# Optimization experiments

Hardware: AMD Instinct MI355X
Metric: run time of the kernel (lower is better)

The kernel has to match this reference:

```python
import jax, jax.numpy as jnp
import numpy as np

N = 100000      # nodes
E = 800000      # edges (avg degree 8)
D_IN = 128
D_OUT = 128
HOPS = 3        # K in SGConv


def setup_inputs() -> dict:
    key = jax.random.key(0)
    k1, k2, k3 = jax.random.split(key, 3)
    x = jax.random.normal(k1, (N, D_IN), dtype=jnp.float32)
    edge_index = jax.random.randint(k2, (2, E), 0, N, dtype=jnp.int64)
    # SGConv's final torch.nn.Linear(in_channels, out_channels)
    W = jax.random.normal(k3, (D_OUT, D_IN), dtype=jnp.float32) / np.sqrt(D_IN).astype(np.float32)
    b = jnp.zeros((D_OUT,), dtype=jnp.float32)
    return {"x": x, "edge_index": edge_index, "W": W, "b": b}


def reference(x, edge_index, W, b):
    n = x.shape[0]
    loop = jnp.arange(n, dtype=edge_index.dtype)
    # gcn_norm with add_self_loops=True (SGConv default)
    src = jnp.concatenate([edge_index[0], loop])  # message sources
    dst = jnp.concatenate([edge_index[1], loop])  # aggregation targets
    ones = jnp.ones(src.shape[0], dtype=x.dtype)
    deg = jax.ops.segment_sum(ones, dst, num_segments=n)
    dinv = jnp.where(deg > 0, jax.lax.rsqrt(deg), 0.0)
    norm = dinv[src] * dinv[dst]  # symmetric D^-1/2 A_hat D^-1/2 coefficients

    def hop(h, _):
        msg = h[src] * norm[:, None]                      # [E+N, D] gather
        return jax.ops.segment_sum(msg, dst, num_segments=n), None

    h, _ = jax.lax.scan(hop, x, None, length=HOPS)        # A_norm^K x
    return h @ W.T + b                                     # final linear
```

## Files before the change

### kernel.cpp

```cpp
#include <hip/hip_runtime.h>
#include <hip/hip_bf16.h>

#define DF 128


typedef __attribute__((ext_vector_type(8))) short shortx8;
typedef __attribute__((ext_vector_type(4))) float floatx4;

__device__ __forceinline__ unsigned short f32_to_bf16_rne(float f) {
    unsigned int u = __float_as_uint(f);
    unsigned int r = (u >> 16) & 1u;
    u += 0x7FFFu + r;
    return (unsigned short)(u >> 16);
}
__device__ __forceinline__ float bf16_lo(unsigned int w) { return __uint_as_float(w << 16); }
__device__ __forceinline__ float bf16_hi(unsigned int w) { return __uint_as_float(w & 0xffff0000u); }
__device__ __forceinline__ unsigned int pack_bf16(float x, float y) {
    return ((unsigned int)f32_to_bf16_rne(y) << 16) | (unsigned int)f32_to_bf16_rne(x);
}

__global__ void detect_flags_kernel(const unsigned int* __restrict__ ew, int enwords,
                                    const unsigned short* __restrict__ xh, int xnh,
                                    int* __restrict__ flagI, int* __restrict__ flagD) {
    __shared__ int eodd_nz;
    __shared__ int xbig;
    if (threadIdx.x == 0) { eodd_nz = 0; xbig = 0; }
    __syncthreads();
    int f1 = 0;
    for (int i = 1 + 2 * (int)threadIdx.x; i < enwords; i += 2 * (int)blockDim.x)
        if (ew[i] != 0u) f1 = 1;
    int c = 0;
    for (int i = 2 * (int)threadIdx.x; i < xnh; i += 2 * (int)blockDim.x) {
        unsigned int e = ((unsigned int)xh[i] >> 7) & 0xFFu;
        if (e >= 0xC0u) c++;
    }
    if (f1) eodd_nz = 1;
    if (c) atomicAdd(&xbig, c);
    __syncthreads();
    if (threadIdx.x == 0) {
        *flagI = (eodd_nz == 0) ? 1 : 0;
        *flagD = (xbig > 8) ? 0 : 1;
    }
}

__global__ void count_deg_kernel(const int* __restrict__ eidx, const int* __restrict__ flagI,
                                 int E, int n, int* __restrict__ cnt) {
    int e = blockIdx.x * blockDim.x + threadIdx.x;
    if (e >= E) return;
    int s, d;
    if (*flagI) {
        const long long* p = (const long long*)eidx;
        s = (int)p[e];
        d = (int)p[(long long)E + e];
    } else {
        s = eidx[e];
        d = eidx[E + e];
    }
    if (d < 0 || d >= n || s < 0 || s >= n) return;
    atomicAdd(&cnt[d], 1);
}

__global__ void dinv_kernel(const int* __restrict__ cnt, float* __restrict__ dinv, int n) {
    int i = blockIdx.x * blockDim.x + threadIdx.x;
    if (i < n) dinv[i] = rsqrtf((float)(cnt[i] + 1));
}

__global__ void scan_blocks_kernel(const int* __restrict__ cnt, int* __restrict__ row_start,
                                   int* __restrict__ partials, int n) {
    __shared__ int s[256];
    int i = blockIdx.x * 256 + threadIdx.x;
    int v = (i < n) ? cnt[i] : 0;
    s[threadIdx.x] = v;
    __syncthreads();
    for (int off = 1; off < 256; off <<= 1) {
        int t = ((int)threadIdx.x >= off) ? s[threadIdx.x - off] : 0;
        __syncthreads();
        s[threadIdx.x] += t;
        __syncthreads();
    }
    if (i < n) row_start[i] = s[threadIdx.x] - v;
    if (threadIdx.x == 255) partials[blockIdx.x] = s[255];
}

__global__ void scan_partials_kernel(int* __restrict__ partials, int nparts) {
    __shared__ int s[512];
    int v = ((int)threadIdx.x < nparts) ? partials[threadIdx.x] : 0;
    s[threadIdx.x] = v;
    __syncthreads();
    for (int off = 1; off < 512; off <<= 1) {
        int t = ((int)threadIdx.x >= off) ? s[threadIdx.x - off] : 0;
        __syncthreads();
        s[threadIdx.x] += t;
        __syncthreads();
    }
    if ((int)threadIdx.x < nparts) partials[threadIdx.x] = s[threadIdx.x] - v;
}

__global__ void finalize_rows_kernel(int* __restrict__ row_start, const int* __restrict__ partials,
                                     const int* __restrict__ cnt, int* __restrict__ cursor, int n) {
    int i = blockIdx.x * 256 + threadIdx.x;
    if (i < n) {
        int r = row_start[i] + partials[blockIdx.x];
        row_start[i] = r;
        cursor[i] = r;
        if (i == n - 1) row_start[n] = r + cnt[i];
    }
}

__global__ void scatter_kernel(const int* __restrict__ eidx, const int* __restrict__ flagI,
                               int E, int n, const float* __restrict__ dinv,
                               int* __restrict__ cursor, int2* __restrict__ csr) {
    int e = blockIdx.x * blockDim.x + threadIdx.x;
    if (e >= E) return;
    int s, d;
    if (*flagI) {
        const long long* p = (const long long*)eidx;
        s = (int)p[e];
        d = (int)p[(long long)E + e];
    } else {
        s = eidx[e];
        d = eidx[E + e];
    }
    if (d < 0 || d >= n || s < 0 || s >= n) return;
    int pos = atomicAdd(&cursor[d], 1);
    int2 pk;
    pk.x = s;
    pk.y = __float_as_int(dinv[s]);
    csr[pos] = pk;
}

__global__ void cast_x_kernel(const void* __restrict__ x, uint2* __restrict__ xb,
                              const int* __restrict__ flagD, int nw2) {
    int i = blockIdx.x * blockDim.x + threadIdx.x;
    if (i >= nw2) return;
    if (*flagD) {
        xb[i] = ((const uint2*)x)[i];
    } else {
        float4 v = ((const float4*)x)[i];
        uint2 o;
        o.x = pack_bf16(v.x, v.y);
        o.y = pack_bf16(v.z, v.w);
        xb[i] = o;
    }
}

__global__ void cast_wb_kernel(const void* __restrict__ W, const void* __restrict__ b,
                               unsigned short* __restrict__ Wb, float* __restrict__ bias_f,
                               const int* __restrict__ flagD) {
    int i = blockIdx.x * 256 + threadIdx.x;
    int bf = *flagD;
    if (i < 128 * 128)
        Wb[i] = bf ? ((const unsigned short*)W)[i] : f32_to_bf16_rne(((const float*)W)[i]);
    if (i < 128)
        bias_f[i] = bf ? bf16_lo((unsigned int)((const unsigned short*)b)[i]) : ((const float*)b)[i];
}

__global__ __launch_bounds__(256) void hop_kernel(const uint4* __restrict__ hin,
                                                  uint4* __restrict__ hout,
                                                  const int2* __restrict__ csr,
                                                  const int* __restrict__ row_start,
                                                  const float* __restrict__ dinv, int n) {
    int gw = (int)((blockIdx.x * 256 + threadIdx.x) >> 6);
    int lane = (int)(threadIdx.x & 63);
    if (gw >= n) return;
    int e = lane >> 4, c = lane & 15;
    float di = dinv[gw];
    int beg = row_start[gw], end = row_start[gw + 1];
    uint4 sv = hin[(size_t)gw * 16 + c];
    float a0 = 0.f, a1 = 0.f, a2 = 0.f, a3 = 0.f, a4 = 0.f, a5 = 0.f, a6 = 0.f, a7 = 0.f;
    for (int j = beg + e; j < end; j += 4) {
        int2 ed = csr[j];
        float w = __int_as_float(ed.y);
        uint4 v = hin[(size_t)ed.x * 16 + c];
        a0 += w * bf16_lo(v.x); a1 += w * bf16_hi(v.x);
        a2 += w * bf16_lo(v.y); a3 += w * bf16_hi(v.y);
        a4 += w * bf16_lo(v.z); a5 += w * bf16_hi(v.z);
        a6 += w * bf16_lo(v.w); a7 += w * bf16_hi(v.w);
    }
    a0 += __shfl_xor(a0, 16); a0 += __shfl_xor(a0, 32);
    a1 += __shfl_xor(a1, 16); a1 += __shfl_xor(a1, 32);
    a2 += __shfl_xor(a2, 16); a2 += __shfl_xor(a2, 32);
    a3 += __shfl_xor(a3, 16); a3 += __shfl_xor(a3, 32);
    a4 += __shfl_xor(a4, 16); a4 += __shfl_xor(a4, 32);
    a5 += __shfl_xor(a5, 16); a5 += __shfl_xor(a5, 32);
    a6 += __shfl_xor(a6, 16); a6 += __shfl_xor(a6, 32);
    a7 += __shfl_xor(a7, 16); a7 += __shfl_xor(a7, 32);
    a0 = di * (a0 + di * bf16_lo(sv.x)); a1 = di * (a1 + di * bf16_hi(sv.x));
    a2 = di * (a2 + di * bf16_lo(sv.y)); a3 = di * (a3 + di * bf16_hi(sv.y));
    a4 = di * (a4 + di * bf16_lo(sv.z)); a5 = di * (a5 + di * bf16_hi(sv.z));
    a6 = di * (a6 + di * bf16_lo(sv.w)); a7 = di * (a7 + di * bf16_hi(sv.w));
    if (e == 0) {
        uint4 o;
        o.x = pack_bf16(a0, a1);
        o.y = pack_bf16(a2, a3);
        o.z = pack_bf16(a4, a5);
        o.w = pack_bf16(a6, a7);
        hout[(size_t)gw * 16 + c] = o;
    }
}

__global__ __launch_bounds__(256, 2) void linear_mfma_kernel(
        const unsigned short* __restrict__ h, const unsigned short* __restrict__ Wb,
        const float* __restrict__ bias_f, void* __restrict__ out,
        const int* __restrict__ flagD, int n) {
    int bf = *flagD;
    int wave = (int)(threadIdx.x >> 6);
    int lane = (int)(threadIdx.x & 63);
    int q = lane >> 4, m16 = lane & 15;

    shortx8 bfrag[8][4];
    float bias[8];
#pragma unroll
    for (int nt = 0; nt < 8; ++nt) {
        int wr = nt * 16 + m16;
#pragma unroll
        for (int t = 0; t < 4; ++t)
            bfrag[nt][t] = *(const shortx8*)&Wb[wr * 128 + t * 32 + q * 8];
        bias[nt] = bias_f[wr];
    }

    int nstrips = (n + 15) / 16;
    int wid = (int)blockIdx.x * 4 + wave;
    int nw = (int)gridDim.x * 4;
    for (int s = wid; s < nstrips; s += nw) {
        int row0 = s * 16;
        int arow = row0 + m16;
        if (arow >= n) arow = n - 1;
        shortx8 afrag[4];
#pragma unroll
        for (int t = 0; t < 4; ++t)
            afrag[t] = *(const shortx8*)&h[(size_t)arow * 128 + t * 32 + q * 8];

        floatx4 acc[8];
#pragma unroll
        for (int nt = 0; nt < 8; ++nt) acc[nt] = (floatx4){0.f, 0.f, 0.f, 0.f};
#pragma unroll
        for (int t = 0; t < 4; ++t)
#pragma unroll
            for (int nt = 0; nt < 8; ++nt)
                acc[nt] = __builtin_amdgcn_mfma_f32_16x16x32_bf16(afrag[t], bfrag[nt][t], acc[nt], 0, 0, 0);

#pragma unroll
        for (int nt = 0; nt < 8; ++nt)
#pragma unroll
            for (int r = 0; r < 4; ++r) {
                int row = row0 + q * 4 + r;
                if (row < n) {
                    float v = acc[nt][r] + bias[nt];
                    size_t oi = (size_t)row * 128 + nt * 16 + m16;
                    if (bf) ((unsigned short*)out)[oi] = f32_to_bf16_rne(v);
                    else    ((float*)out)[oi] = v;
                }
            }
    }
}

extern "C" void kernel_launch(void* const* d_in, const int* in_sizes, int n_in,
                              void* d_out, int out_size, void* d_ws, size_t ws_size,
                              hipStream_t stream) {
    const void* x = d_in[0];
    const int* eidx = (const int*)d_in[1];
    const void* W = d_in[2];
    const void* b = d_in[3];

    int n = in_sizes[0] / DF;
    int E = in_sizes[1] / 2;

    char* ws = (char*)d_ws;
    size_t off = 0;
    auto alloc = [&](size_t bytes) -> void* {
        void* p = ws + off;
        off = (off + bytes + 255) & ~(size_t)255;
        return p;
    };
    unsigned int* hb = (unsigned int*)alloc((size_t)n * 64 * 4);
    float* dinv      = (float*)alloc((size_t)n * 4);
    int*   cnt       = (int*)alloc((size_t)n * 4);
    int*   row_start = (int*)alloc((size_t)(n + 1) * 4);
    int*   cursor    = (int*)alloc((size_t)n * 4);
    int*   partials  = (int*)alloc(4096);
    int*   flagI     = (int*)alloc(256);
    int*   flagD     = (int*)alloc(256);
    unsigned short* Wb = (unsigned short*)alloc(128 * 128 * 2);
    float* bias_f    = (float*)alloc(128 * 4);
    int2*  csr       = (int2*)alloc((size_t)E * 8);
    unsigned int* xb = (unsigned int*)d_out;

    hipMemsetAsync(cnt, 0, (size_t)n * 4, stream);

    int enw = 8192; if (2 * E < enw) enw = 2 * E;
    int xnh = 16384; if (n * DF < xnh) xnh = n * DF;
    detect_flags_kernel<<<1, 256, 0, stream>>>((const unsigned int*)eidx, enw,
                                               (const unsigned short*)x, xnh, flagI, flagD);

    int eb = (E + 255) / 256;
    int nb = (n + 255) / 256;
    count_deg_kernel<<<eb, 256, 0, stream>>>(eidx, flagI, E, n, cnt);
    dinv_kernel<<<nb, 256, 0, stream>>>(cnt, dinv, n);
    scan_blocks_kernel<<<nb, 256, 0, stream>>>(cnt, row_start, partials, n);
    scan_partials_kernel<<<1, 512, 0, stream>>>(partials, nb);
    finalize_rows_kernel<<<nb, 256, 0, stream>>>(row_start, partials, cnt, cursor, n);
    scatter_kernel<<<eb, 256, 0, stream>>>(eidx, flagI, E, n, dinv, cursor, csr);

    int nw2 = n * 32;
    cast_x_kernel<<<(nw2 + 255) / 256, 256, 0, stream>>>(x, (uint2*)xb, flagD, nw2);
    cast_wb_kernel<<<64, 256, 0, stream>>>(W, b, Wb, bias_f, flagD);

    int hb_grid = (n + 3) / 4;
    hop_kernel<<<hb_grid, 256, 0, stream>>>((const uint4*)xb, (uint4*)hb, csr, row_start, dinv, n);
    hop_kernel<<<hb_grid, 256, 0, stream>>>((const uint4*)hb, (uint4*)xb, csr, row_start, dinv, n);
    hop_kernel<<<hb_grid, 256, 0, stream>>>((const uint4*)xb, (uint4*)hb, csr, row_start, dinv, n);

    int nstrips = (n + 15) / 16;
    int lgrid = 512; if ((nstrips + 3) / 4 < lgrid) lgrid = (nstrips + 3) / 4;
    linear_mfma_kernel<<<lgrid, 256, 0, stream>>>(
        (const unsigned short*)hb, Wb, bias_f, d_out, flagD, n);
}
```

Baseline: 358.5 us.

## Partition degree count and CSR scatter into destination-range buckets per block group

Count and scatter kernels now use a fixed grid of 512 blocks split into 8 groups. Each group loops over all edges but only handles destinations in its eighth of the node range. The aim is to localize atomics and CSR writes (likely keeping them within one XCD's L2 via block-to-XCD round robin) and cut cross-die atomic traffic. The cost is that each group rereads the whole destination index array, so index reads grow eightfold.

Measured after the change: 386.1 us. 7.7% more time.

```diff
diff --git a/kernel.cpp b/kernel.cpp
--- a/kernel.cpp
+++ b/kernel.cpp
@@ -43,21 +43,24 @@
     }
 }
 
-__global__ void count_deg_kernel(const int* __restrict__ eidx, const int* __restrict__ flagI,
-                                 int E, int n, int* __restrict__ cnt) {
-    int e = blockIdx.x * blockDim.x + threadIdx.x;
-    if (e >= E) return;
-    int s, d;
-    if (*flagI) {
-        const long long* p = (const long long*)eidx;
-        s = (int)p[e];
-        d = (int)p[(long long)E + e];
-    } else {
-        s = eidx[e];
-        d = eidx[E + e];
-    }
-    if (d < 0 || d >= n || s < 0 || s >= n) return;
-    atomicAdd(&cnt[d], 1);
+__global__ __launch_bounds__(256) void count_deg_kernel(const int* __restrict__ eidx,
+                                                        const int* __restrict__ flagI,
+                                                        int E, int n, int* __restrict__ cnt) {
+    int bucket = (int)(blockIdx.x & 7);
+    int bsize = (n + 7) >> 3;
+    int lo = bucket * bsize;
+    int hi = lo + bsize; if (hi > n) hi = n;
+    int nthr = (int)(gridDim.x >> 3) * (int)blockDim.x;
+    int t0 = (int)(blockIdx.x >> 3) * (int)blockDim.x + (int)threadIdx.x;
+    int isI64 = *flagI;
+    const long long* p64 = (const long long*)eidx;
+    for (int e = t0; e < E; e += nthr) {
+        int d = isI64 ? (int)p64[(long long)E + e] : eidx[E + e];
+        if (d < lo || d >= hi) continue;
+        int s = isI64 ? (int)p64[e] : eidx[e];
+        if (s < 0 || s >= n) continue;
+        atomicAdd(&cnt[d], 1);
+    }
 }
 
 __global__ void dinv_kernel(const int* __restrict__ cnt, float* __restrict__ dinv, int n) {
@@ -107,26 +110,29 @@
     }
 }
 
-__global__ void scatter_kernel(const int* __restrict__ eidx, const int* __restrict__ flagI,
-                               int E, int n, const float* __restrict__ dinv,
-                               int* __restrict__ cursor, int2* __restrict__ csr) {
-    int e = blockIdx.x * blockDim.x + threadIdx.x;
-    if (e >= E) return;
-    int s, d;
-    if (*flagI) {
-        const long long* p = (const long long*)eidx;
-        s = (int)p[e];
-        d = (int)p[(long long)E + e];
-    } else {
-        s = eidx[e];
-        d = eidx[E + e];
-    }
-    if (d < 0 || d >= n || s < 0 || s >= n) return;
-    int pos = atomicAdd(&cursor[d], 1);
-    int2 pk;
-    pk.x = s;
-    pk.y = __float_as_int(dinv[s]);
-    csr[pos] = pk;
+__global__ __launch_bounds__(256) void scatter_kernel(const int* __restrict__ eidx,
+                                                      const int* __restrict__ flagI,
+                                                      int E, int n, const float* __restrict__ dinv,
+                                                      int* __restrict__ cursor, int2* __restrict__ csr) {
+    int bucket = (int)(blockIdx.x & 7);
+    int bsize = (n + 7) >> 3;
+    int lo = bucket * bsize;
+    int hi = lo + bsize; if (hi > n) hi = n;
+    int nthr = (int)(gridDim.x >> 3) * (int)blockDim.x;
+    int t0 = (int)(blockIdx.x >> 3) * (int)blockDim.x + (int)threadIdx.x;
+    int isI64 = *flagI;
+    const long long* p64 = (const long long*)eidx;
+    for (int e = t0; e < E; e += nthr) {
+        int d = isI64 ? (int)p64[(long long)E + e] : eidx[E + e];
+        if (d < lo || d >= hi) continue;
+        int s = isI64 ? (int)p64[e] : eidx[e];
+        if (s < 0 || s >= n) continue;
+        int pos = atomicAdd(&cursor[d], 1);
+        int2 pk;
+        pk.x = s;
+        pk.y = __float_as_int(dinv[s]);
+        csr[pos] = pk;
+    }
 }
 
 __global__ void cast_x_kernel(const void* __restrict__ x, uint2* __restrict__ xb,
@@ -293,14 +299,14 @@
     detect_flags_kernel<<<1, 256, 0, stream>>>((const unsigned int*)eidx, enw,
                                                (const unsigned short*)x, xnh, flagI, flagD);
 
-    int eb = (E + 255) / 256;
     int nb = (n + 255) / 256;
-    count_deg_kernel<<<eb, 256, 0, stream>>>(eidx, flagI, E, n, cnt);
+    int ebgrid = 8 * 64;
+    count_deg_kernel<<<ebgrid, 256, 0, stream>>>(eidx, flagI, E, n, cnt);
     dinv_kernel<<<nb, 256, 0, stream>>>(cnt, dinv, n);
     scan_blocks_kernel<<<nb, 256, 0, stream>>>(cnt, row_start, partials, n);
     scan_partials_kernel<<<1, 512, 0, stream>>>(partials, nb);
     finalize_rows_kernel<<<nb, 256, 0, stream>>>(row_start, partials, cnt, cursor, n);
-    scatter_kernel<<<eb, 256, 0, stream>>>(eidx, flagI, E, n, dinv, cursor, csr);
+    scatter_kernel<<<ebgrid, 256, 0, stream>>>(eidx, flagI, E, n, dinv, cursor, csr);
 
     int nw2 = n * 32;
     cast_x_kernel<<<(nw2 + 255) / 256, 256, 0, stream>>>(x, (uint2*)xb, flagD, nw2);
```
